# Performance work log

Measured on AMD Instinct MI355X. Metric: run time of the kernel, lower is better.

The kernel has to match this reference:

```python
import jax, jax.numpy as jnp
import numpy as np

SCALE = 8.0  # sqrt(d_k=64)


def setup_inputs() -> dict:
    key = jax.random.key(0)
    kq, kk, kv, km = jax.random.split(key, 4)
    B, L, D = 8, 4096, 64
    q = jax.random.normal(kq, (B, L, D), dtype=jnp.float32)
    k = jax.random.normal(kk, (B, L, D), dtype=jnp.float32)
    v = jax.random.normal(kv, (B, L, D), dtype=jnp.float32)
    mask = jax.random.randint(km, (B, L, L), 0, 2) == 1  # True = masked out
    return {"q": q, "k": k, "v": v, "mask": mask}


def reference(q, k, v, mask):
    # scores: [B, Lq, Lk]
    u = jnp.einsum('bqd,bkd->bqk', q, k) / SCALE
    u = jnp.where(mask, -jnp.inf, u)
    attn = jax.nn.softmax(u, axis=2)
    output = jnp.einsum('bqk,bkd->bqd', attn, v)
    return (attn, output)
```

## Files before the change

### kernel.cpp

```cpp
#include <hip/hip_runtime.h>
#include <hip/hip_bf16.h>
#include <stdint.h>

#define BB 8
#define LL 4096
#define DD 64
#define KT 64
#define NT (LL / KT)

typedef short bf16x8 __attribute__((ext_vector_type(8)));
typedef short bf16x4 __attribute__((ext_vector_type(4)));
typedef short bf16x2 __attribute__((ext_vector_type(2)));
typedef float f32x4 __attribute__((ext_vector_type(4)));

__device__ inline short f2bfs(float x) {
    __hip_bfloat16 h = __float2bfloat16(x);
    return __builtin_bit_cast(short, h);
}

__device__ inline bf16x8 pack8v(f32x4 a, f32x4 b) {
    bf16x8 r;
    r[0] = f2bfs(a[0]); r[1] = f2bfs(a[1]); r[2] = f2bfs(a[2]); r[3] = f2bfs(a[3]);
    r[4] = f2bfs(b[0]); r[5] = f2bfs(b[1]); r[6] = f2bfs(b[2]); r[7] = f2bfs(b[3]);
    return r;
}

__device__ inline int swzf(int r) { return (r & 7) ^ ((r >> 3) & 7); }

__global__ void detect_mask_kernel(const uint32_t* __restrict__ w, uint32_t* __restrict__ flag) {
    __shared__ int nonbin;
    if (threadIdx.x == 0) nonbin = 0;
    __syncthreads();
    int bad = 0;
    for (int i = threadIdx.x; i < 4096; i += 256) bad |= (w[i] > 1u) ? 1 : 0;
    if (bad) atomicOr(&nonbin, 1);
    __syncthreads();
    if (threadIdx.x == 0) *flag = (uint32_t)(nonbin != 0);
}

__global__ __launch_bounds__(512, 4) void fused_attn_kernel(
    const float* __restrict__ qg, const float* __restrict__ kg,
    const float* __restrict__ vg, const void* __restrict__ maskv,
    const uint32_t* __restrict__ flagp,
    float* __restrict__ attn, float* __restrict__ outp)
{
    __shared__ alignas(16) ushort Kt[2][KT * 64];
    __shared__ alignas(16) ushort Vt[2][64 * KT];
    __shared__ alignas(16) ushort Ps[64 * KT];
    __shared__ uint8_t Msk[8][NT][64];

    const int tid = (int)threadIdx.x;
    const int w   = tid >> 6, l = tid & 63;
    const int lr  = l & 15, lg = l >> 4;
    const int rg  = w & 3, ch = w >> 2;
    const int id  = (int)blockIdx.x;
    const int b   = id & 7;
    const int q0  = (id >> 3) * 64;
    const bool mbyte = (*flagp != 0);

    const float* kb = kg + (size_t)b * LL * DD;
    const float* vb = vg + (size_t)b * LL * DD;

    const int qrow = q0 + 16 * rg + lr;
    const uint8_t* mrow8  = (const uint8_t*)maskv + (size_t)b * LL * LL + (size_t)qrow * LL + ch * 32 + lg * 4;
    const int*     mrow32 = (const int*)maskv     + (size_t)b * LL * LL + (size_t)qrow * LL + ch * 32 + lg * 4;
    float* arow = attn + (size_t)b * LL * LL + (size_t)qrow * LL + ch * 32 + lg * 4;

    bf16x8 qf0, qf1;
    {
        const float* qp = qg + (size_t)(b * LL + qrow) * DD + lg * 8;
        qf0 = pack8v(*(const f32x4*)(qp)      * 0.125f, *(const f32x4*)(qp + 4)  * 0.125f);
        qf1 = pack8v(*(const f32x4*)(qp + 32) * 0.125f, *(const f32x4*)(qp + 36) * 0.125f);
    }

    const int krow0 = tid >> 3, kc8 = tid & 7;
    f32x4 ka0, ka1;
    auto kissue = [&](int kbase) {
        const float* p = kb + (size_t)(kbase + krow0) * DD + kc8 * 8;
        ka0 = *(const f32x4*)p;
        ka1 = *(const f32x4*)(p + 4);
    };
    auto kcommit = [&](int buf) {
        *(bf16x8*)&Kt[buf][krow0 * 64 + ((kc8 ^ swzf(krow0)) << 3)] = pack8v(ka0, ka1);
    };

    const int vk2 = tid >> 4, vd4 = tid & 15;
    f32x4 va0, va1;
    auto vissue = [&](int kbase) {
        const float* p = vb + (size_t)(kbase + vk2 * 2) * DD + vd4 * 4;
        va0 = *(const f32x4*)p;
        va1 = *(const f32x4*)(p + DD);
    };
    auto vcommit = [&](int buf) {
        const int k0 = vk2 * 2;
        #pragma unroll
        for (int e = 0; e < 4; ++e) {
            const int d = vd4 * 4 + e;
            bf16x2 t;
            t[0] = f2bfs(va0[e]);
            t[1] = f2bfs(va1[e]);
            *(bf16x2*)&Vt[buf][d * 64 + ((((k0 >> 3) ^ swzf(d))) << 3) + (k0 & 7)] = t;
        }
    };

    float rsum = 0.f;
    uint32_t mw0 = 0, mw1 = 0;
    if (mbyte) {
        mw0 = *(const uint32_t*)(mrow8);
        mw1 = *(const uint32_t*)(mrow8 + 16);
    }
    kissue(0); kcommit(0);
    __syncthreads();
    #pragma unroll 1
    for (int kt = 0; kt < NT; ++kt) {
        const int cur = kt & 1, kbase = kt * KT;
        const bool more = (kt < NT - 1);
        if (more) kissue(kbase + KT);
        uint32_t nw0 = 0, nw1 = 0;
        if (mbyte && more) {
            nw0 = *(const uint32_t*)(mrow8 + kbase + KT);
            nw1 = *(const uint32_t*)(mrow8 + kbase + KT + 16);
        }
        uint32_t mbits = 0;
        #pragma unroll
        for (int n = 0; n < 2; ++n) {
            const int krow = ch * 32 + n * 16 + lr;
            bf16x8 k0 = *(const bf16x8*)&Kt[cur][krow * 64 + ((lg       ^ swzf(krow)) << 3)];
            bf16x8 k1 = *(const bf16x8*)&Kt[cur][krow * 64 + (((4 + lg) ^ swzf(krow)) << 3)];
            f32x4 c = {0.f, 0.f, 0.f, 0.f};
            c = __builtin_amdgcn_mfma_f32_16x16x32_bf16(k0, qf0, c, 0, 0, 0);
            c = __builtin_amdgcn_mfma_f32_16x16x32_bf16(k1, qf1, c, 0, 0, 0);
            if (mbyte) {
                const uint32_t mwc = n ? mw1 : mw0;
                #pragma unroll
                for (int j = 0; j < 4; ++j) {
                    const uint32_t mk = (mwc >> (8 * j)) & 0xffu;
                    mbits |= (mk ? 1u : 0u) << (n * 4 + j);
                    rsum += mk ? 0.f : __expf(c[j]);
                }
            } else {
                const int4 mi = *(const int4*)(mrow32 + kbase + n * 16);
                const int mk[4] = {mi.x, mi.y, mi.z, mi.w};
                #pragma unroll
                for (int j = 0; j < 4; ++j) {
                    mbits |= (mk[j] ? 1u : 0u) << (n * 4 + j);
                    rsum += mk[j] ? 0.f : __expf(c[j]);
                }
            }
        }
        Msk[w][kt][l] = (uint8_t)mbits;
        mw0 = nw0; mw1 = nw1;
        if (more) kcommit((kt + 1) & 1);
        __syncthreads();
    }

    rsum += __shfl_xor(rsum, 16, 64);
    rsum += __shfl_xor(rsum, 32, 64);
    float* Rs = (float*)Ps;
    if (lg == 0) Rs[ch * 64 + 16 * rg + lr] = rsum;
    __syncthreads();
    const float rinv = 1.0f / (Rs[16 * rg + lr] + Rs[64 + 16 * rg + lr]);

    f32x4 oacc0 = {0.f, 0.f, 0.f, 0.f}, oacc1 = {0.f, 0.f, 0.f, 0.f};
    kissue(0); vissue(0);
    kcommit(0); vcommit(0);
    __syncthreads();
    #pragma unroll 1
    for (int kt = 0; kt < NT; ++kt) {
        const int cur = kt & 1, kbase = kt * KT;
        const bool more = (kt < NT - 1);
        if (more) { kissue(kbase + KT); vissue(kbase + KT); }
        const int mb = (int)Msk[w][kt][l];
        const int prow = 16 * rg + lr;
        #pragma unroll
        for (int n = 0; n < 2; ++n) {
            const int krow = ch * 32 + n * 16 + lr;
            bf16x8 k0 = *(const bf16x8*)&Kt[cur][krow * 64 + ((lg       ^ swzf(krow)) << 3)];
            bf16x8 k1 = *(const bf16x8*)&Kt[cur][krow * 64 + (((4 + lg) ^ swzf(krow)) << 3)];
            f32x4 c = {0.f, 0.f, 0.f, 0.f};
            c = __builtin_amdgcn_mfma_f32_16x16x32_bf16(k0, qf0, c, 0, 0, 0);
            c = __builtin_amdgcn_mfma_f32_16x16x32_bf16(k1, qf1, c, 0, 0, 0);
            f32x4 pv;
            #pragma unroll
            for (int j = 0; j < 4; ++j)
                pv[j] = ((mb >> (n * 4 + j)) & 1) ? 0.f : __expf(c[j]) * rinv;
            *(f32x4*)(arow + kbase + n * 16) = pv;
            bf16x4 pb;
            pb[0] = f2bfs(pv[0]); pb[1] = f2bfs(pv[1]);
            pb[2] = f2bfs(pv[2]); pb[3] = f2bfs(pv[3]);
            const int chunk = ch * 4 + n * 2 + (lg >> 1);
            *(bf16x4*)&Ps[prow * 64 + ((chunk ^ swzf(prow)) << 3) + (lg & 1) * 4] = pb;
        }
        __syncthreads();

        {
            bf16x8 pa[2];
            #pragma unroll
            for (int ks = 0; ks < 2; ++ks)
                pa[ks] = *(const bf16x8*)&Ps[prow * 64 + ((((ks << 2) + lg) ^ swzf(prow)) << 3)];
            const int d0 = ch * 32 + lr;
            const int d1 = d0 + 16;
            #pragma unroll
            for (int ks = 0; ks < 2; ++ks) {
                bf16x8 vf = *(const bf16x8*)&Vt[cur][d0 * 64 + ((((ks << 2) + lg) ^ swzf(d0)) << 3)];
                oacc0 = __builtin_amdgcn_mfma_f32_16x16x32_bf16(pa[ks], vf, oacc0, 0, 0, 0);
            }
            #pragma unroll
            for (int ks = 0; ks < 2; ++ks) {
                bf16x8 vf = *(const bf16x8*)&Vt[cur][d1 * 64 + ((((ks << 2) + lg) ^ swzf(d1)) << 3)];
                oacc1 = __builtin_amdgcn_mfma_f32_16x16x32_bf16(pa[ks], vf, oacc1, 0, 0, 0);
            }
        }

        if (more) { kcommit((kt + 1) & 1); vcommit((kt + 1) & 1); }
        __syncthreads();
    }

    #pragma unroll
    for (int r = 0; r < 4; ++r) {
        const size_t orow = (size_t)(b * LL + q0 + 16 * rg + lg * 4 + r) * DD;
        outp[orow + ch * 32 + lr]      = oacc0[r];
        outp[orow + ch * 32 + 16 + lr] = oacc1[r];
    }
}

extern "C" void kernel_launch(void* const* d_in, const int* in_sizes, int n_in,
                              void* d_out, int out_size, void* d_ws, size_t ws_size,
                              hipStream_t stream) {
    const float* q = (const float*)d_in[0];
    const float* k = (const float*)d_in[1];
    const float* v = (const float*)d_in[2];
    const void* mask = d_in[3];
    float* attn = (float*)d_out;
    float* outp = attn + (size_t)BB * LL * LL;
    uint32_t* flagp = (uint32_t*)d_ws;

    detect_mask_kernel<<<1, 256, 0, stream>>>((const uint32_t*)mask, flagp);
    fused_attn_kernel<<<dim3((LL / 64) * BB), 512, 0, stream>>>(q, k, v, mask, flagp, attn, outp);
}
```

Baseline: 385.8 us.

## Compute P·V in first pass with unnormalized probabilities; simplify attn-write second pass

Moves the P·V MFMA into the first (row-sum) pass using unnormalized exp values packed directly into registers, then normalizes the output at the end. A cross-wave LDS reduction combines the two column-half partial outputs. The second pass now only recomputes scores and writes attn, over 128-key double-buffered K tiles with nontemporal stores. It also remaps K rows so each lane's 8 contiguous attn/mask columns match an MFMA operand, which removes the Ps LDS round trip and one barrier per tile, at the cost of V loads in pass one and extra registers for four accumulators.

Result: slower. 485.9 us (+25.9%).

```diff
diff --git a/kernel.cpp b/kernel.cpp
--- a/kernel.cpp
+++ b/kernel.cpp
@@ -7,9 +7,9 @@
 #define DD 64
 #define KT 64
 #define NT (LL / KT)
+#define NP2 (LL / 128)
 
 typedef short bf16x8 __attribute__((ext_vector_type(8)));
-typedef short bf16x4 __attribute__((ext_vector_type(4)));
 typedef short bf16x2 __attribute__((ext_vector_type(2)));
 typedef float f32x4 __attribute__((ext_vector_type(4)));
 
@@ -25,7 +25,8 @@
     return r;
 }
 
-__device__ inline int swzf(int r) { return (r & 7) ^ ((r >> 3) & 7); }
+__device__ inline int swzK(int r) { return (r & 3) | (((r >> 3) & 1) << 2); }
+__device__ inline int swzV(int r) { return (r & 7) ^ ((r >> 3) & 7); }
 
 __global__ void detect_mask_kernel(const uint32_t* __restrict__ w, uint32_t* __restrict__ flag) {
     __shared__ int nonbin;
@@ -44,10 +45,9 @@
     const uint32_t* __restrict__ flagp,
     float* __restrict__ attn, float* __restrict__ outp)
 {
-    __shared__ alignas(16) ushort Kt[2][KT * 64];
-    __shared__ alignas(16) ushort Vt[2][64 * KT];
-    __shared__ alignas(16) ushort Ps[64 * KT];
+    __shared__ alignas(16) ushort KB[4][KT * 64];
     __shared__ uint8_t Msk[8][NT][64];
+    __shared__ float Rs[128];
 
     const int tid = (int)threadIdx.x;
     const int w   = tid >> 6, l = tid & 63;
@@ -62,9 +62,9 @@
     const float* vb = vg + (size_t)b * LL * DD;
 
     const int qrow = q0 + 16 * rg + lr;
-    const uint8_t* mrow8  = (const uint8_t*)maskv + (size_t)b * LL * LL + (size_t)qrow * LL + ch * 32 + lg * 4;
-    const int*     mrow32 = (const int*)maskv     + (size_t)b * LL * LL + (size_t)qrow * LL + ch * 32 + lg * 4;
-    float* arow = attn + (size_t)b * LL * LL + (size_t)qrow * LL + ch * 32 + lg * 4;
+    const uint8_t* mrow8  = (const uint8_t*)maskv + (size_t)b * LL * LL + (size_t)qrow * LL + ch * 32 + lg * 8;
+    const int*     mrow32 = (const int*)maskv     + (size_t)b * LL * LL + (size_t)qrow * LL + ch * 32 + lg * 8;
+    float* arow = attn + (size_t)b * LL * LL + (size_t)qrow * LL + ch * 32 + lg * 8;
 
     bf16x8 qf0, qf1;
     {
@@ -75,23 +75,22 @@
 
     const int krow0 = tid >> 3, kc8 = tid & 7;
     f32x4 ka0, ka1;
-    auto kissue = [&](int kbase) {
+    auto kiss1 = [&](int kbase) {
         const float* p = kb + (size_t)(kbase + krow0) * DD + kc8 * 8;
         ka0 = *(const f32x4*)p;
         ka1 = *(const f32x4*)(p + 4);
     };
-    auto kcommit = [&](int buf) {
-        *(bf16x8*)&Kt[buf][krow0 * 64 + ((kc8 ^ swzf(krow0)) << 3)] = pack8v(ka0, ka1);
-    };
-
+    auto kcom1 = [&](int buf) {
+        *(bf16x8*)&KB[buf][krow0 * 64 + ((kc8 ^ swzK(krow0)) << 3)] = pack8v(ka0, ka1);
+    };
     const int vk2 = tid >> 4, vd4 = tid & 15;
     f32x4 va0, va1;
-    auto vissue = [&](int kbase) {
+    auto viss = [&](int kbase) {
         const float* p = vb + (size_t)(kbase + vk2 * 2) * DD + vd4 * 4;
         va0 = *(const f32x4*)p;
         va1 = *(const f32x4*)(p + DD);
     };
-    auto vcommit = [&](int buf) {
+    auto vcom = [&](int buf) {
         const int k0 = vk2 * 2;
         #pragma unroll
         for (int e = 0; e < 4; ++e) {
@@ -99,128 +98,150 @@
             bf16x2 t;
             t[0] = f2bfs(va0[e]);
             t[1] = f2bfs(va1[e]);
-            *(bf16x2*)&Vt[buf][d * 64 + ((((k0 >> 3) ^ swzf(d))) << 3) + (k0 & 7)] = t;
+            *(bf16x2*)&KB[2 + buf][d * 64 + (((k0 >> 3) ^ swzV(d)) << 3) + (k0 & 7)] = t;
         }
     };
 
     float rsum = 0.f;
-    uint32_t mw0 = 0, mw1 = 0;
-    if (mbyte) {
-        mw0 = *(const uint32_t*)(mrow8);
-        mw1 = *(const uint32_t*)(mrow8 + 16);
-    }
-    kissue(0); kcommit(0);
+    f32x4 oacc[4];
+    #pragma unroll
+    for (int g = 0; g < 4; ++g) { f32x4 z = {0.f, 0.f, 0.f, 0.f}; oacc[g] = z; }
+
+    uint64_t mw = 0;
+    int4 mi0 = {0,0,0,0}, mi1 = {0,0,0,0};
+    if (mbyte) mw = *(const uint64_t*)(mrow8);
+    else { mi0 = *(const int4*)(mrow32); mi1 = *(const int4*)(mrow32 + 4); }
+
+    kiss1(0); viss(0);
+    kcom1(0); vcom(0);
     __syncthreads();
     #pragma unroll 1
     for (int kt = 0; kt < NT; ++kt) {
         const int cur = kt & 1, kbase = kt * KT;
         const bool more = (kt < NT - 1);
-        if (more) kissue(kbase + KT);
-        uint32_t nw0 = 0, nw1 = 0;
-        if (mbyte && more) {
-            nw0 = *(const uint32_t*)(mrow8 + kbase + KT);
-            nw1 = *(const uint32_t*)(mrow8 + kbase + KT + 16);
-        }
+        if (more) { kiss1(kbase + KT); viss(kbase + KT); }
+        uint64_t nmw = 0;
+        int4 ni0 = {0,0,0,0}, ni1 = {0,0,0,0};
+        if (more) {
+            if (mbyte) nmw = *(const uint64_t*)(mrow8 + kbase + KT);
+            else { ni0 = *(const int4*)(mrow32 + kbase + KT); ni1 = *(const int4*)(mrow32 + kbase + KT + 4); }
+        }
+
         uint32_t mbits = 0;
+        float p8[8];
         #pragma unroll
         for (int n = 0; n < 2; ++n) {
-            const int krow = ch * 32 + n * 16 + lr;
-            bf16x8 k0 = *(const bf16x8*)&Kt[cur][krow * 64 + ((lg       ^ swzf(krow)) << 3)];
-            bf16x8 k1 = *(const bf16x8*)&Kt[cur][krow * 64 + (((4 + lg) ^ swzf(krow)) << 3)];
+            const int krow = ch * 32 + ((lr >> 2) << 3) + (n << 2) + (lr & 3);
+            bf16x8 k0 = *(const bf16x8*)&KB[cur][krow * 64 + ((lg       ^ swzK(krow)) << 3)];
+            bf16x8 k1 = *(const bf16x8*)&KB[cur][krow * 64 + (((4 + lg) ^ swzK(krow)) << 3)];
             f32x4 c = {0.f, 0.f, 0.f, 0.f};
             c = __builtin_amdgcn_mfma_f32_16x16x32_bf16(k0, qf0, c, 0, 0, 0);
             c = __builtin_amdgcn_mfma_f32_16x16x32_bf16(k1, qf1, c, 0, 0, 0);
-            if (mbyte) {
-                const uint32_t mwc = n ? mw1 : mw0;
-                #pragma unroll
-                for (int j = 0; j < 4; ++j) {
-                    const uint32_t mk = (mwc >> (8 * j)) & 0xffu;
-                    mbits |= (mk ? 1u : 0u) << (n * 4 + j);
-                    rsum += mk ? 0.f : __expf(c[j]);
+            #pragma unroll
+            for (int j = 0; j < 4; ++j) {
+                const int t = n * 4 + j;
+                int mk;
+                if (mbyte) mk = (int)((mw >> (8 * t)) & 0xffu);
+                else {
+                    const int4 mi = n ? mi1 : mi0;
+                    mk = (j == 0) ? mi.x : (j == 1) ? mi.y : (j == 2) ? mi.z : mi.w;
                 }
-            } else {
-                const int4 mi = *(const int4*)(mrow32 + kbase + n * 16);
-                const int mk[4] = {mi.x, mi.y, mi.z, mi.w};
-                #pragma unroll
-                for (int j = 0; j < 4; ++j) {
-                    mbits |= (mk[j] ? 1u : 0u) << (n * 4 + j);
-                    rsum += mk[j] ? 0.f : __expf(c[j]);
-                }
+                mbits |= (mk ? 1u : 0u) << t;
+                const float pv = mk ? 0.f : __expf(c[j]);
+                rsum += pv;
+                p8[t] = pv;
             }
         }
         Msk[w][kt][l] = (uint8_t)mbits;
-        mw0 = nw0; mw1 = nw1;
-        if (more) kcommit((kt + 1) & 1);
+
+        bf16x8 pa;
+        #pragma unroll
+        for (int t = 0; t < 8; ++t) pa[t] = f2bfs(p8[t]);
+
+        #pragma unroll
+        for (int g = 0; g < 4; ++g) {
+            const int d = g * 16 + lr;
+            bf16x8 vf = *(const bf16x8*)&KB[2 + cur][d * 64 + (((ch * 4 + lg) ^ swzV(d)) << 3)];
+            oacc[g] = __builtin_amdgcn_mfma_f32_16x16x32_bf16(pa, vf, oacc[g], 0, 0, 0);
+        }
+
+        mw = nmw; mi0 = ni0; mi1 = ni1;
+        if (more) { kcom1((kt + 1) & 1); vcom((kt + 1) & 1); }
         __syncthreads();
     }
 
     rsum += __shfl_xor(rsum, 16, 64);
     rsum += __shfl_xor(rsum, 32, 64);
-    float* Rs = (float*)Ps;
     if (lg == 0) Rs[ch * 64 + 16 * rg + lr] = rsum;
     __syncthreads();
     const float rinv = 1.0f / (Rs[16 * rg + lr] + Rs[64 + 16 * rg + lr]);
 
-    f32x4 oacc0 = {0.f, 0.f, 0.f, 0.f}, oacc1 = {0.f, 0.f, 0.f, 0.f};
-    kissue(0); vissue(0);
-    kcommit(0); vcommit(0);
+    f32x4 kA[4];
+    auto kiss2 = [&](int kbase) {
+        #pragma unroll
+        for (int m = 0; m < 2; ++m) {
+            const float* p = kb + (size_t)(kbase + krow0 + 64 * m) * DD + kc8 * 8;
+            kA[2 * m]     = *(const f32x4*)p;
+            kA[2 * m + 1] = *(const f32x4*)(p + 4);
+        }
+    };
+    auto kcom2 = [&](int pair) {
+        #pragma unroll
+        for (int m = 0; m < 2; ++m)
+            *(bf16x8*)&KB[2 * pair + m][krow0 * 64 + ((kc8 ^ swzK(krow0)) << 3)] = pack8v(kA[2 * m], kA[2 * m + 1]);
+    };
+
+    kiss2(0); kcom2(0);
     __syncthreads();
     #pragma unroll 1
-    for (int kt = 0; kt < NT; ++kt) {
-        const int cur = kt & 1, kbase = kt * KT;
-        const bool more = (kt < NT - 1);
-        if (more) { kissue(kbase + KT); vissue(kbase + KT); }
-        const int mb = (int)Msk[w][kt][l];
-        const int prow = 16 * rg + lr;
-        #pragma unroll
-        for (int n = 0; n < 2; ++n) {
-            const int krow = ch * 32 + n * 16 + lr;
-            bf16x8 k0 = *(const bf16x8*)&Kt[cur][krow * 64 + ((lg       ^ swzf(krow)) << 3)];
-            bf16x8 k1 = *(const bf16x8*)&Kt[cur][krow * 64 + (((4 + lg) ^ swzf(krow)) << 3)];
-            f32x4 c = {0.f, 0.f, 0.f, 0.f};
-            c = __builtin_amdgcn_mfma_f32_16x16x32_bf16(k0, qf0, c, 0, 0, 0);
-            c = __builtin_amdgcn_mfma_f32_16x16x32_bf16(k1, qf1, c, 0, 0, 0);
-            f32x4 pv;
+    for (int kt2 = 0; kt2 < NP2; ++kt2) {
+        const int pair = kt2 & 1, kbase2 = kt2 * 128;
+        const bool more = (kt2 < NP2 - 1);
+        if (more) kiss2(kbase2 + 128);
+        #pragma unroll
+        for (int h = 0; h < 2; ++h) {
+            const int mb = (int)Msk[w][2 * kt2 + h][l];
+            const ushort* Kbuf = KB[2 * pair + h];
+            #pragma unroll
+            for (int n = 0; n < 2; ++n) {
+                const int krow = ch * 32 + ((lr >> 2) << 3) + (n << 2) + (lr & 3);
+                bf16x8 k0 = *(const bf16x8*)&Kbuf[krow * 64 + ((lg       ^ swzK(krow)) << 3)];
+                bf16x8 k1 = *(const bf16x8*)&Kbuf[krow * 64 + (((4 + lg) ^ swzK(krow)) << 3)];
+                f32x4 c = {0.f, 0.f, 0.f, 0.f};
+                c = __builtin_amdgcn_mfma_f32_16x16x32_bf16(k0, qf0, c, 0, 0, 0);
+                c = __builtin_amdgcn_mfma_f32_16x16x32_bf16(k1, qf1, c, 0, 0, 0);
+                f32x4 pv;
+                #pragma unroll
+                for (int j = 0; j < 4; ++j)
+                    pv[j] = ((mb >> (n * 4 + j)) & 1) ? 0.f : __expf(c[j]) * rinv;
+                __builtin_nontemporal_store(pv, (f32x4*)(arow + kbase2 + h * 64 + n * 4));
+            }
+        }
+        if (more) kcom2((kt2 + 1) & 1);
+        __syncthreads();
+    }
+
+    float* OutL = (float*)KB;
+    if (ch == 1) {
+        #pragma unroll
+        for (int g = 0; g < 4; ++g)
             #pragma unroll
             for (int j = 0; j < 4; ++j)
-                pv[j] = ((mb >> (n * 4 + j)) & 1) ? 0.f : __expf(c[j]) * rinv;
-            *(f32x4*)(arow + kbase + n * 16) = pv;
-            bf16x4 pb;
-            pb[0] = f2bfs(pv[0]); pb[1] = f2bfs(pv[1]);
-            pb[2] = f2bfs(pv[2]); pb[3] = f2bfs(pv[3]);
-            const int chunk = ch * 4 + n * 2 + (lg >> 1);
-            *(bf16x4*)&Ps[prow * 64 + ((chunk ^ swzf(prow)) << 3) + (lg & 1) * 4] = pb;
-        }
-        __syncthreads();
-
-        {
-            bf16x8 pa[2];
-            #pragma unroll
-            for (int ks = 0; ks < 2; ++ks)
-                pa[ks] = *(const bf16x8*)&Ps[prow * 64 + ((((ks << 2) + lg) ^ swzf(prow)) << 3)];
-            const int d0 = ch * 32 + lr;
-            const int d1 = d0 + 16;
-            #pragma unroll
-            for (int ks = 0; ks < 2; ++ks) {
-                bf16x8 vf = *(const bf16x8*)&Vt[cur][d0 * 64 + ((((ks << 2) + lg) ^ swzf(d0)) << 3)];
-                oacc0 = __builtin_amdgcn_mfma_f32_16x16x32_bf16(pa[ks], vf, oacc0, 0, 0, 0);
+                OutL[rg * 1088 + (lg * 4 + j) * 68 + g * 16 + lr] = oacc[g][j];
+    }
+    __syncthreads();
+    if (ch == 0) {
+        #pragma unroll
+        for (int j = 0; j < 4; ++j) {
+            const int ql = 16 * rg + lg * 4 + j;
+            const float ri = 1.0f / (Rs[ql] + Rs[64 + ql]);
+            const size_t orow = (size_t)(b * LL + q0 + ql) * DD;
+            #pragma unroll
+            for (int g = 0; g < 4; ++g) {
+                const float o = (oacc[g][j] + OutL[rg * 1088 + (lg * 4 + j) * 68 + g * 16 + lr]) * ri;
+                __builtin_nontemporal_store(o, &outp[orow + g * 16 + lr]);
             }
-            #pragma unroll
-            for (int ks = 0; ks < 2; ++ks) {
-                bf16x8 vf = *(const bf16x8*)&Vt[cur][d1 * 64 + ((((ks << 2) + lg) ^ swzf(d1)) << 3)];
-                oacc1 = __builtin_amdgcn_mfma_f32_16x16x32_bf16(pa[ks], vf, oacc1, 0, 0, 0);
-            }
-        }
-
-        if (more) { kcommit((kt + 1) & 1); vcommit((kt + 1) & 1); }
-        __syncthreads();
-    }
-
-    #pragma unroll
-    for (int r = 0; r < 4; ++r) {
-        const size_t orow = (size_t)(b * LL + q0 + 16 * rg + lg * 4 + r) * DD;
-        outp[orow + ch * 32 + lr]      = oacc0[r];
-        outp[orow + ch * 32 + 16 + lr] = oacc1[r];
+        }
     }
 }
 
```
